# Optimization experiments

Hardware: AMD Instinct MI355X
Metric: run time of the kernel (lower is better)

The kernel has to match this reference:

```python
import jax, jax.numpy as jnp
import numpy as np

B, L, D_MODEL, N_HEADS = 2, 2048, 1024, 16
D_HEAD = D_MODEL // N_HEADS


def setup_inputs() -> dict:
    key = jax.random.key(0)
    k0, k1, k2 = jax.random.split(key, 3)
    x = jax.random.normal(k0, (B, L, D_MODEL), dtype=jnp.float32)
    qkv_w = jax.random.normal(k1, (3 * D_MODEL, D_MODEL), dtype=jnp.float32) * 0.02
    qkv_b = jnp.zeros((3 * D_MODEL,), dtype=jnp.float32)
    o_w = jax.random.normal(k2, (D_MODEL, D_MODEL), dtype=jnp.float32) * 0.02
    o_b = jnp.zeros((D_MODEL,), dtype=jnp.float32)
    attn_mask = jnp.ones((B, 1, L, L), dtype=jnp.int32)  # 1 = visible
    return {"x": x, "qkv_w": qkv_w, "qkv_b": qkv_b, "o_w": o_w, "o_b": o_b, "attn_mask": attn_mask}


def _rope(x, sin, cos):
    half = x.shape[-1] // 2
    x1, x2 = x[..., :half], x[..., half:]
    return jnp.concatenate([x1 * cos - x2 * sin, x1 * sin + x2 * cos], axis=-1)


def reference(x, qkv_w, qkv_b, o_w, o_b, attn_mask):
    Bx, Lx, D = x.shape
    H, Dh = N_HEADS, D // N_HEADS
    qkv = x @ qkv_w.T + qkv_b                          # (B, L, 3D)
    qkv = qkv.reshape(Bx, Lx, 3, H, Dh).transpose(2, 0, 3, 1, 4)  # (3, B, H, L, Dh)
    q, k, v = qkv[0], qkv[1], qkv[2]
    # RoPE: freq_i = 1/10000^(2i/Dh) over first half of head dim
    half = Dh // 2
    freq = 1.0 / (10000.0 ** (2.0 * jnp.arange(half, dtype=jnp.float32) / Dh))
    t = jnp.arange(Lx, dtype=jnp.float32)
    freqs = t[:, None] * freq[None, :]                 # (L, half)
    sin, cos = jnp.sin(freqs), jnp.cos(freqs)
    q, k = _rope(q, sin, cos), _rope(k, sin, cos)
    scores = jnp.einsum('bhqd,bhkd->bhqk', q, k) / jnp.sqrt(jnp.float32(Dh))
    causal = jnp.tril(jnp.ones((Lx, Lx), dtype=bool))  # (L, L)
    neg_inf = jnp.float32(-jnp.inf)
    scores = jnp.where(causal[None, None], scores, neg_inf)
    scores = jnp.where(attn_mask == 0, neg_inf, scores)
    probs = jax.nn.softmax(scores, axis=-1)
    ctx = jnp.einsum('bhqk,bhkd->bhqd', probs, v)      # (B, H, L, Dh)
    ctx = ctx.transpose(0, 2, 1, 3).reshape(Bx, Lx, D)
    return ctx @ o_w.T + o_b
```

## Files before the change

### kernel.cpp

```cpp
#include <hip/hip_runtime.h>

#define Bz 2
#define Lz 2048
#define Dm 1024
#define Hh 16
#define Dh 64

typedef float f32x4 __attribute__((ext_vector_type(4)));
typedef short bf16x8 __attribute__((ext_vector_type(8)));
typedef short bf16x4 __attribute__((ext_vector_type(4)));

typedef __attribute__((address_space(1))) void GV;
typedef __attribute__((address_space(3))) void LV;

#if defined(__has_builtin)
#if __has_builtin(__builtin_amdgcn_mfma_f32_16x16x16bf16_1k)
#define HAVE_MFMA16 1
#endif
#if __has_builtin(__builtin_amdgcn_exp2f)
#define EXP2(x) __builtin_amdgcn_exp2f(x)
#endif
#endif
#ifndef EXP2
#define EXP2(x) exp2f(x)
#endif

#define QSCALE 0.18033688011112042f

__device__ __forceinline__ short f2bf(float f) {
    union { float f; unsigned int u; } c; c.f = f;
    unsigned int u = c.u;
    unsigned int r = (u + 0x7fffu + ((u >> 16) & 1u)) >> 16;
    return (short)r;
}

__global__ __launch_bounds__(256) void cvt_all(
    const float* __restrict__ x, const float* __restrict__ qw,
    const float* __restrict__ ow, unsigned short* __restrict__ xb,
    unsigned short* __restrict__ qwb, unsigned short* __restrict__ owb)
{
    int u = blockIdx.x * 256 + threadIdx.x;
    const float* in; unsigned short* out; int off;
    if (u < 524288)       { in = x;  out = xb;  off = u; }
    else if (u < 917504)  { in = qw; out = qwb; off = u - 524288; }
    else                  { in = ow; out = owb; off = u - 917504; }
    const float4 f0 = *reinterpret_cast<const float4*>(in + (size_t)off * 8);
    const float4 f1 = *reinterpret_cast<const float4*>(in + (size_t)off * 8 + 4);
    bf16x8 o;
    o[0] = f2bf(f0.x); o[1] = f2bf(f0.y); o[2] = f2bf(f0.z); o[3] = f2bf(f0.w);
    o[4] = f2bf(f1.x); o[5] = f2bf(f1.y); o[6] = f2bf(f1.z); o[7] = f2bf(f1.w);
    *reinterpret_cast<bf16x8*>(out + (size_t)off * 8) = o;
}

template <int MODE>
__global__ __launch_bounds__(256) void gemm_bt_bf16(
    const unsigned short* __restrict__ A, const unsigned short* __restrict__ W,
    const float* __restrict__ bias, void* __restrict__ Cv,
    unsigned short* __restrict__ Vt, int N, int K)
{
    __shared__ __align__(16) unsigned short At[128 * 32];
    __shared__ __align__(16) unsigned short Wt[128 * 32];

    const int lane = threadIdx.x & 63;
    const int wv = threadIdx.x >> 6;
    const int wm = wv >> 1, wn = wv & 1;
    const int r = lane & 15, q4 = lane >> 4;
    const int m0 = blockIdx.y * 128;
    const int n0 = blockIdx.x * 128;

    const int srow = lane >> 2;
    const int sk = (lane & 3) * 8;

    f32x4 acc[4][4] = {};

    const unsigned short* Abase = A + (size_t)(m0 + wv * 32 + srow) * K + sk;
    const unsigned short* Wbase = W + (size_t)(n0 + wv * 32 + srow) * K + sk;

    for (int k0 = 0; k0 < K; k0 += 32) {
        __syncthreads();
#pragma unroll
        for (int j = 0; j < 2; j++) {
            __builtin_amdgcn_global_load_lds(
                (GV*)(Abase + (size_t)j * 16 * K + k0),
                (LV*)&At[(wv * 32 + j * 16) * 32], 16, 0, 0);
            __builtin_amdgcn_global_load_lds(
                (GV*)(Wbase + (size_t)j * 16 * K + k0),
                (LV*)&Wt[(wv * 32 + j * 16) * 32], 16, 0, 0);
        }
        __syncthreads();

        bf16x8 af[4], bfr[4];
#pragma unroll
        for (int mi = 0; mi < 4; mi++)
            af[mi] = *reinterpret_cast<bf16x8*>(&At[(wm * 64 + mi * 16 + r) * 32 + q4 * 8]);
#pragma unroll
        for (int ni = 0; ni < 4; ni++)
            bfr[ni] = *reinterpret_cast<bf16x8*>(&Wt[(wn * 64 + ni * 16 + r) * 32 + q4 * 8]);
#pragma unroll
        for (int mi = 0; mi < 4; mi++)
#pragma unroll
            for (int ni = 0; ni < 4; ni++)
                acc[mi][ni] = __builtin_amdgcn_mfma_f32_16x16x32_bf16(af[mi], bfr[ni], acc[mi][ni], 0, 0, 0);
    }

    if constexpr (MODE == 2) {
        const int colbase = n0 + wn * 64;
        if (colbase >= 2048) {
            const int hh = (colbase - 2048) >> 6;
#pragma unroll
            for (int mi = 0; mi < 4; mi++) {
                const int row0 = m0 + wm * 64 + mi * 16 + q4 * 4;
                const int bb = row0 >> 11;
                const int lc = (row0 & 2047) >> 2;
#pragma unroll
                for (int ni = 0; ni < 4; ni++) {
                    const int dd = ni * 16 + r;
                    const float bv = bias[colbase + ni * 16 + r];
                    ushort4 st;
                    st.x = (unsigned short)f2bf(acc[mi][ni][0] + bv);
                    st.y = (unsigned short)f2bf(acc[mi][ni][1] + bv);
                    st.z = (unsigned short)f2bf(acc[mi][ni][2] + bv);
                    st.w = (unsigned short)f2bf(acc[mi][ni][3] + bv);
                    *reinterpret_cast<ushort4*>(
                        &Vt[((size_t)((bb * 16 + hh) * 512 + lc)) * 256 + dd * 4]) = st;
                }
            }
        } else {
            const float qs = (colbase < 1024) ? QSCALE : 1.0f;
            unsigned short* qko = (unsigned short*)Cv;
#pragma unroll
            for (int np = 0; np < 2; np++) {
                const int d = np * 16 + r;
                const float fr = exp2f(-(float)d * 0.41524101186092029f);
                const float sf = sinf(fr), cf = cosf(fr);
                const float blo = bias[colbase + np * 16 + r];
                const float bhi = bias[colbase + np * 16 + r + 32];
#pragma unroll
                for (int mi = 0; mi < 4; mi++) {
                    const int row0 = m0 + wm * 64 + mi * 16 + q4 * 4;
                    const int l0 = row0 & 2047;
                    float ang = (float)l0 * fr;
                    float s = sinf(ang), c = cosf(ang);
#pragma unroll
                    for (int reg = 0; reg < 4; reg++) {
                        float x1 = acc[mi][np][reg] + blo;
                        float x2 = acc[mi][np + 2][reg] + bhi;
                        float olo = (x1 * c - x2 * s) * qs;
                        float ohi = (x1 * s + x2 * c) * qs;
                        size_t rowoff = (size_t)(row0 + reg) * 2048 + colbase + np * 16 + r;
                        qko[rowoff] = (unsigned short)f2bf(olo);
                        qko[rowoff + 32] = (unsigned short)f2bf(ohi);
                        float s2 = s * cf + c * sf;
                        c = c * cf - s * sf;
                        s = s2;
                    }
                }
            }
        }
    } else {
#pragma unroll
        for (int mi = 0; mi < 4; mi++)
#pragma unroll
            for (int ni = 0; ni < 4; ni++) {
                int col = n0 + wn * 64 + ni * 16 + r;
                float bv = bias[col];
#pragma unroll
                for (int reg = 0; reg < 4; reg++) {
                    int row = m0 + wm * 64 + mi * 16 + q4 * 4 + reg;
                    ((float*)Cv)[(size_t)row * N + col] = acc[mi][ni][reg] + bv;
                }
            }
    }
}

__global__ __launch_bounds__(256) void attn_kernel(
    const unsigned short* __restrict__ qk, const unsigned short* __restrict__ Vt,
    unsigned short* __restrict__ ctx)
{
    const int n = blockIdx.x;
    const int bh = (n & 7) | (((n >> 3) & 3) << 3);
    const int pr = n >> 5;
    const int b = bh >> 4, h = bh & 15;
    const int w = threadIdx.x >> 6;
    const int lane = threadIdx.x & 63;
    const int r = lane & 15, q4 = lane >> 4;

    __shared__ __align__(16) unsigned short Kbuf[64 * 64];
    __shared__ __align__(16) unsigned short Vbuf[64 * 64];
#ifndef HAVE_MFMA16
    __shared__ __align__(16) unsigned short Pl[4][16][72];
#endif

    const unsigned short* kg =
        qk + ((size_t)(b * Lz + w * 16 + (lane >> 3))) * 2048 + 1024 + h * 64
           + (((lane & 7) ^ (lane >> 3)) * 8);
    const unsigned short* vg =
        Vt + ((size_t)(bh * 512 + w * 4 + (lane >> 5))) * 256 + (lane & 31) * 8;

#pragma unroll
    for (int phase = 0; phase < 2; phase++) {
        const int qi = phase ? (31 - pr) : pr;
        const int qb = qi * 64;
        const int wq = qb + w * 16;

        const unsigned short* qptr = qk + ((size_t)(b * Lz + wq + r)) * 2048 + h * 64;
        bf16x8 qf[2];
        qf[0] = *reinterpret_cast<const bf16x8*>(qptr + q4 * 8);
        qf[1] = *reinterpret_cast<const bf16x8*>(qptr + 32 + q4 * 8);

        f32x4 o[4] = {};
        float l_i = 0.f;

        const int ntiles = qi + 1;
        for (int it = 0; it < ntiles; ++it) {
            const int k0 = it * 64;
            __syncthreads();
#pragma unroll
            for (int half = 0; half < 2; half++) {
                __builtin_amdgcn_global_load_lds(
                    (GV*)(kg + (size_t)(k0 + half * 8) * 2048),
                    (LV*)&Kbuf[(w * 16 + half * 8) * 64], 16, 0, 0);
                __builtin_amdgcn_global_load_lds(
                    (GV*)(vg + (size_t)((k0 >> 2) + half * 2) * 256),
                    (LV*)&Vbuf[(w * 4 + half * 2) * 256], 16, 0, 0);
            }
            __syncthreads();

            f32x4 S[4] = {};
#pragma unroll
            for (int ns = 0; ns < 4; ns++)
#pragma unroll
                for (int ks = 0; ks < 2; ks++) {
                    bf16x8 kf = *reinterpret_cast<bf16x8*>(
                        &Kbuf[(ns * 16 + r) * 64 + (((ks * 4 + q4) ^ (r & 7)) * 8)]);
                    S[ns] = __builtin_amdgcn_mfma_f32_16x16x32_bf16(kf, qf[ks], S[ns], 0, 0, 0);
                }

            if (k0 + 63 > wq) {
#pragma unroll
                for (int ns = 0; ns < 4; ns++) {
                    int key = k0 + ns * 16 + q4 * 4;
#pragma unroll
                    for (int reg = 0; reg < 4; reg++)
                        if (key + reg > wq + r) S[ns][reg] = -1e30f;
                }
            }

            float sum = 0.f;
#pragma unroll
            for (int ns = 0; ns < 4; ns++)
#pragma unroll
                for (int reg = 0; reg < 4; reg++) {
                    S[ns][reg] = EXP2(S[ns][reg]);
                    sum += S[ns][reg];
                }
            sum += __shfl_xor(sum, 16);
            sum += __shfl_xor(sum, 32);
            l_i += sum;

#ifdef HAVE_MFMA16
            bf16x4 pf[4];
#pragma unroll
            for (int ns = 0; ns < 4; ns++) {
                bf16x4 p;
#pragma unroll
                for (int reg = 0; reg < 4; reg++) p[reg] = f2bf(S[ns][reg]);
                pf[ns] = p;
            }
#pragma unroll
            for (int ns = 0; ns < 4; ns++)
#pragma unroll
                for (int dt = 0; dt < 4; dt++) {
                    bf16x4 vf = *reinterpret_cast<bf16x4*>(
                        &Vbuf[((ns * 4 + q4) * 64 + dt * 16 + r) * 4]);
                    o[dt] = __builtin_amdgcn_mfma_f32_16x16x16bf16_1k(vf, pf[ns], o[dt], 0, 0, 0);
                }
#else
#pragma unroll
            for (int ns = 0; ns < 4; ns++)
#pragma unroll
                for (int reg = 0; reg < 4; reg++)
                    Pl[w][r][ns * 16 + q4 * 4 + reg] = (unsigned short)f2bf(S[ns][reg]);
#pragma unroll
            for (int ks32 = 0; ks32 < 2; ks32++) {
                bf16x8 pf8 = *reinterpret_cast<bf16x8*>(&Pl[w][r][ks32 * 32 + q4 * 8]);
#pragma unroll
                for (int dt = 0; dt < 4; dt++) {
                    bf16x4 vlo = *reinterpret_cast<bf16x4*>(
                        &Vbuf[((ks32 * 8 + q4 * 2) * 64 + dt * 16 + r) * 4]);
                    bf16x4 vhi = *reinterpret_cast<bf16x4*>(
                        &Vbuf[((ks32 * 8 + q4 * 2 + 1) * 64 + dt * 16 + r) * 4]);
                    bf16x8 vf8;
                    vf8[0] = vlo[0]; vf8[1] = vlo[1]; vf8[2] = vlo[2]; vf8[3] = vlo[3];
                    vf8[4] = vhi[0]; vf8[5] = vhi[1]; vf8[6] = vhi[2]; vf8[7] = vhi[3];
                    o[dt] = __builtin_amdgcn_mfma_f32_16x16x32_bf16(vf8, pf8, o[dt], 0, 0, 0);
                }
            }
#endif
        }

        float rl = 1.0f / l_i;
        unsigned short* cp =
            ctx + ((size_t)(b * Lz + wq + r)) * Dm + h * 64 + q4 * 4;
#pragma unroll
        for (int dt = 0; dt < 4; dt++) {
            ushort4 st;
            st.x = (unsigned short)f2bf(o[dt][0] * rl);
            st.y = (unsigned short)f2bf(o[dt][1] * rl);
            st.z = (unsigned short)f2bf(o[dt][2] * rl);
            st.w = (unsigned short)f2bf(o[dt][3] * rl);
            *reinterpret_cast<ushort4*>(cp + dt * 16) = st;
        }
    }
}

extern "C" void kernel_launch(void* const* d_in, const int* in_sizes, int n_in,
                              void* d_out, int out_size, void* d_ws, size_t ws_size,
                              hipStream_t stream)
{
    const float* x     = (const float*)d_in[0];
    const float* qkv_w = (const float*)d_in[1];
    const float* qkv_b = (const float*)d_in[2];
    const float* o_w   = (const float*)d_in[3];
    const float* o_b   = (const float*)d_in[4];

    char* ws = (char*)d_ws;
    unsigned short* xb   = (unsigned short*)(ws);
    unsigned short* qwb  = (unsigned short*)(ws + ( 8u << 20));
    unsigned short* owb  = (unsigned short*)(ws + (14u << 20));
    unsigned short* qkb  = (unsigned short*)(ws + (16u << 20));
    unsigned short* Vtb  = (unsigned short*)(ws + (32u << 20));
    unsigned short* ctxb = (unsigned short*)(ws + (40u << 20));
    float* out = (float*)d_out;

    cvt_all<<<4096, 256, 0, stream>>>(x, qkv_w, o_w, xb, qwb, owb);
    gemm_bt_bf16<2><<<dim3(24, 32), 256, 0, stream>>>(xb, qwb, qkv_b, qkb, Vtb, 3072, 1024);
    attn_kernel<<<512, 256, 0, stream>>>(qkb, Vtb, ctxb);
    gemm_bt_bf16<0><<<dim3(8, 32), 256, 0, stream>>>(ctxb, owb, o_b, out, nullptr, 1024, 1024);
}
```

Before: 206.2 us.

## Deepen GEMM K-tile with XOR-swizzled LDS, add RoPE table, narrow output tiles

Raises the GEMM K step from 32 to 64 and stores it in LDS with an XOR swizzle to avoid bank conflicts. This halves the number of barrier pairs per K loop. A sin/cos table is precomputed in the conversion kernel so the QKV epilogue reads it instead of calling sinf/cosf per row. The output projection uses 64-wide N tiles to launch twice as many blocks and improve CU occupancy. The costs are more LDS per block and an extra table write and read.

```diff
diff --git a/kernel.cpp b/kernel.cpp
--- a/kernel.cpp
+++ b/kernel.cpp
@@ -37,70 +37,88 @@
 __global__ __launch_bounds__(256) void cvt_all(
     const float* __restrict__ x, const float* __restrict__ qw,
     const float* __restrict__ ow, unsigned short* __restrict__ xb,
-    unsigned short* __restrict__ qwb, unsigned short* __restrict__ owb)
+    unsigned short* __restrict__ qwb, unsigned short* __restrict__ owb,
+    float2* __restrict__ tab)
 {
     int u = blockIdx.x * 256 + threadIdx.x;
-    const float* in; unsigned short* out; int off;
-    if (u < 524288)       { in = x;  out = xb;  off = u; }
-    else if (u < 917504)  { in = qw; out = qwb; off = u - 524288; }
-    else                  { in = ow; out = owb; off = u - 917504; }
-    const float4 f0 = *reinterpret_cast<const float4*>(in + (size_t)off * 8);
-    const float4 f1 = *reinterpret_cast<const float4*>(in + (size_t)off * 8 + 4);
-    bf16x8 o;
-    o[0] = f2bf(f0.x); o[1] = f2bf(f0.y); o[2] = f2bf(f0.z); o[3] = f2bf(f0.w);
-    o[4] = f2bf(f1.x); o[5] = f2bf(f1.y); o[6] = f2bf(f1.z); o[7] = f2bf(f1.w);
-    *reinterpret_cast<bf16x8*>(out + (size_t)off * 8) = o;
-}
-
-template <int MODE>
+    if (u < 1048576) {
+        const float* in; unsigned short* out; int off;
+        if (u < 524288)       { in = x;  out = xb;  off = u; }
+        else if (u < 917504)  { in = qw; out = qwb; off = u - 524288; }
+        else                  { in = ow; out = owb; off = u - 917504; }
+        const float4 f0 = *reinterpret_cast<const float4*>(in + (size_t)off * 8);
+        const float4 f1 = *reinterpret_cast<const float4*>(in + (size_t)off * 8 + 4);
+        bf16x8 o;
+        o[0] = f2bf(f0.x); o[1] = f2bf(f0.y); o[2] = f2bf(f0.z); o[3] = f2bf(f0.w);
+        o[4] = f2bf(f1.x); o[5] = f2bf(f1.y); o[6] = f2bf(f1.z); o[7] = f2bf(f1.w);
+        *reinterpret_cast<bf16x8*>(out + (size_t)off * 8) = o;
+    } else {
+        int t = u - 1048576;
+        int l = t >> 5, d = t & 31;
+        float fr = exp2f(-(float)d * 0.41524101186092029f);
+        float ang = (float)l * fr;
+        tab[t] = make_float2(sinf(ang), cosf(ang));
+    }
+}
+
+template <int MODE, int TN>
 __global__ __launch_bounds__(256) void gemm_bt_bf16(
     const unsigned short* __restrict__ A, const unsigned short* __restrict__ W,
     const float* __restrict__ bias, void* __restrict__ Cv,
-    unsigned short* __restrict__ Vt, int N, int K)
+    unsigned short* __restrict__ Vt, const float2* __restrict__ tab, int N, int K)
 {
-    __shared__ __align__(16) unsigned short At[128 * 32];
-    __shared__ __align__(16) unsigned short Wt[128 * 32];
+    constexpr int NB = (TN == 128) ? 4 : 2;
+    __shared__ __align__(16) unsigned short At[128 * 64];
+    __shared__ __align__(16) unsigned short Wt[TN * 64];
 
     const int lane = threadIdx.x & 63;
     const int wv = threadIdx.x >> 6;
     const int wm = wv >> 1, wn = wv & 1;
     const int r = lane & 15, q4 = lane >> 4;
     const int m0 = blockIdx.y * 128;
-    const int n0 = blockIdx.x * 128;
-
-    const int srow = lane >> 2;
-    const int sk = (lane & 3) * 8;
-
-    f32x4 acc[4][4] = {};
-
-    const unsigned short* Abase = A + (size_t)(m0 + wv * 32 + srow) * K + sk;
-    const unsigned short* Wbase = W + (size_t)(n0 + wv * 32 + srow) * K + sk;
-
-    for (int k0 = 0; k0 < K; k0 += 32) {
+    const int n0 = blockIdx.x * TN;
+
+    const int srow8 = lane >> 3;
+    const int skS = (((lane & 7) ^ srow8) * 8);
+
+    f32x4 acc[4][NB] = {};
+
+    const unsigned short* Abase = A + (size_t)(m0 + wv * 32 + srow8) * K + skS;
+    const unsigned short* Wbase =
+        W + (size_t)(n0 + wv * (TN / 4) + srow8) * K + skS;
+
+    for (int k0 = 0; k0 < K; k0 += 64) {
         __syncthreads();
 #pragma unroll
-        for (int j = 0; j < 2; j++) {
+        for (int j = 0; j < 4; j++)
             __builtin_amdgcn_global_load_lds(
-                (GV*)(Abase + (size_t)j * 16 * K + k0),
-                (LV*)&At[(wv * 32 + j * 16) * 32], 16, 0, 0);
+                (GV*)(Abase + (size_t)(j * 8) * K + k0),
+                (LV*)&At[(wv * 32 + j * 8) * 64], 16, 0, 0);
+#pragma unroll
+        for (int j = 0; j < TN / 32; j++)
             __builtin_amdgcn_global_load_lds(
-                (GV*)(Wbase + (size_t)j * 16 * K + k0),
-                (LV*)&Wt[(wv * 32 + j * 16) * 32], 16, 0, 0);
+                (GV*)(Wbase + (size_t)(j * 8) * K + k0),
+                (LV*)&Wt[(wv * (TN / 4) + j * 8) * 64], 16, 0, 0);
+        __syncthreads();
+
+#pragma unroll
+        for (int ks = 0; ks < 2; ks++) {
+            const int ch = ((ks * 4 + q4) ^ (r & 7)) * 8;
+            bf16x8 af[4], bfr[NB];
+#pragma unroll
+            for (int mi = 0; mi < 4; mi++)
+                af[mi] = *reinterpret_cast<bf16x8*>(&At[(wm * 64 + mi * 16 + r) * 64 + ch]);
+#pragma unroll
+            for (int ni = 0; ni < NB; ni++)
+                bfr[ni] = *reinterpret_cast<bf16x8*>(
+                    &Wt[(wn * (TN / 2) + ni * 16 + r) * 64 + ch]);
+#pragma unroll
+            for (int mi = 0; mi < 4; mi++)
+#pragma unroll
+                for (int ni = 0; ni < NB; ni++)
+                    acc[mi][ni] = __builtin_amdgcn_mfma_f32_16x16x32_bf16(
+                        af[mi], bfr[ni], acc[mi][ni], 0, 0, 0);
         }
-        __syncthreads();
-
-        bf16x8 af[4], bfr[4];
-#pragma unroll
-        for (int mi = 0; mi < 4; mi++)
-            af[mi] = *reinterpret_cast<bf16x8*>(&At[(wm * 64 + mi * 16 + r) * 32 + q4 * 8]);
-#pragma unroll
-        for (int ni = 0; ni < 4; ni++)
-            bfr[ni] = *reinterpret_cast<bf16x8*>(&Wt[(wn * 64 + ni * 16 + r) * 32 + q4 * 8]);
-#pragma unroll
-        for (int mi = 0; mi < 4; mi++)
-#pragma unroll
-            for (int ni = 0; ni < 4; ni++)
-                acc[mi][ni] = __builtin_amdgcn_mfma_f32_16x16x32_bf16(af[mi], bfr[ni], acc[mi][ni], 0, 0, 0);
     }
 
     if constexpr (MODE == 2) {
@@ -131,16 +149,15 @@
 #pragma unroll
             for (int np = 0; np < 2; np++) {
                 const int d = np * 16 + r;
-                const float fr = exp2f(-(float)d * 0.41524101186092029f);
-                const float sf = sinf(fr), cf = cosf(fr);
+                const float2 rot = tab[32 + d];
                 const float blo = bias[colbase + np * 16 + r];
                 const float bhi = bias[colbase + np * 16 + r + 32];
 #pragma unroll
                 for (int mi = 0; mi < 4; mi++) {
                     const int row0 = m0 + wm * 64 + mi * 16 + q4 * 4;
                     const int l0 = row0 & 2047;
-                    float ang = (float)l0 * fr;
-                    float s = sinf(ang), c = cosf(ang);
+                    const float2 sc = tab[l0 * 32 + d];
+                    float s = sc.x, c = sc.y;
 #pragma unroll
                     for (int reg = 0; reg < 4; reg++) {
                         float x1 = acc[mi][np][reg] + blo;
@@ -150,8 +167,8 @@
                         size_t rowoff = (size_t)(row0 + reg) * 2048 + colbase + np * 16 + r;
                         qko[rowoff] = (unsigned short)f2bf(olo);
                         qko[rowoff + 32] = (unsigned short)f2bf(ohi);
-                        float s2 = s * cf + c * sf;
-                        c = c * cf - s * sf;
+                        float s2 = s * rot.y + c * rot.x;
+                        c = c * rot.y - s * rot.x;
                         s = s2;
                     }
                 }
@@ -161,8 +178,8 @@
 #pragma unroll
         for (int mi = 0; mi < 4; mi++)
 #pragma unroll
-            for (int ni = 0; ni < 4; ni++) {
-                int col = n0 + wn * 64 + ni * 16 + r;
+            for (int ni = 0; ni < NB; ni++) {
+                int col = n0 + wn * (TN / 2) + ni * 16 + r;
                 float bv = bias[col];
 #pragma unroll
                 for (int reg = 0; reg < 4; reg++) {
@@ -331,10 +348,13 @@
     unsigned short* qkb  = (unsigned short*)(ws + (16u << 20));
     unsigned short* Vtb  = (unsigned short*)(ws + (32u << 20));
     unsigned short* ctxb = (unsigned short*)(ws + (40u << 20));
+    float2* tab          = (float2*)(ws + (48u << 20));
     float* out = (float*)d_out;
 
-    cvt_all<<<4096, 256, 0, stream>>>(x, qkv_w, o_w, xb, qwb, owb);
-    gemm_bt_bf16<2><<<dim3(24, 32), 256, 0, stream>>>(xb, qwb, qkv_b, qkb, Vtb, 3072, 1024);
+    cvt_all<<<4352, 256, 0, stream>>>(x, qkv_w, o_w, xb, qwb, owb, tab);
+    gemm_bt_bf16<2, 128><<<dim3(24, 32), 256, 0, stream>>>(
+        xb, qwb, qkv_b, qkb, Vtb, tab, 3072, 1024);
     attn_kernel<<<512, 256, 0, stream>>>(qkb, Vtb, ctxb);
-    gemm_bt_bf16<0><<<dim3(8, 32), 256, 0, stream>>>(ctxb, owb, o_b, out, nullptr, 1024, 1024);
-}
+    gemm_bt_bf16<0, 64><<<dim3(16, 32), 256, 0, stream>>>(
+        ctxb, owb, o_b, out, nullptr, nullptr, 1024, 1024);
+}
```

Result: no change. 203.2 us (-1.4%).
